# Optimization experiments

Hardware: AMD Instinct MI355X
Metric: run time of the kernel (lower is better)

The kernel has to match this reference:

```python
import jax, jax.numpy as jnp
import numpy as np

POOL = 7          # cf.pool_size
SR = 2            # roi_align sampling_ratio
LEVELS = [0, 1, 2, 3]
C = 192           # cf.end_filts
HC = 2            # cf.head_classes
RF = 1
N_ROIS = 1000
B = 4


def roi_align_2d(fmap, boxes, batch_inds, pool_size=POOL, sr=SR):
    """Bilinear RoIAlign. fmap [B,C,H,W]; boxes [N,4] = (y1,x1,y2,x2) in fmap pixel coords."""
    _, _, H, W = fmap.shape
    y1, x1, y2, x2 = boxes[:, 0], boxes[:, 1], boxes[:, 2], boxes[:, 3]
    bin_h = jnp.maximum(y2 - y1, 1.0) / pool_size
    bin_w = jnp.maximum(x2 - x1, 1.0) / pool_size
    # sampling offsets within the roi, [pool*sr]
    grid = (jnp.arange(pool_size, dtype=jnp.float32)[:, None]
            + (jnp.arange(sr, dtype=jnp.float32)[None, :] + 0.5) / sr).reshape(-1)
    ys = y1[:, None] + grid[None, :] * bin_h[:, None]   # [N, P*S]
    xs = x1[:, None] + grid[None, :] * bin_w[:, None]   # [N, P*S]
    y = jnp.broadcast_to(ys[:, :, None], (ys.shape[0], ys.shape[1], xs.shape[1]))  # [N,PS,PS]
    x = jnp.broadcast_to(xs[:, None, :], y.shape)
    valid = (y >= -1.0) & (y <= H) & (x >= -1.0) & (x <= W)
    y = jnp.clip(y, 0.0, H - 1)
    x = jnp.clip(x, 0.0, W - 1)
    y0 = jnp.floor(y).astype(jnp.int32)
    x0 = jnp.floor(x).astype(jnp.int32)
    y1i = jnp.minimum(y0 + 1, H - 1)
    x1i = jnp.minimum(x0 + 1, W - 1)
    ly = y - y0
    lx = x - x0
    b = batch_inds[:, None, None]
    f00 = fmap[b, :, y0, x0]    # [N,PS,PS,C]
    f01 = fmap[b, :, y0, x1i]
    f10 = fmap[b, :, y1i, x0]
    f11 = fmap[b, :, y1i, x1i]
    w00 = ((1 - ly) * (1 - lx))[..., None]
    w01 = ((1 - ly) * lx)[..., None]
    w10 = (ly * (1 - lx))[..., None]
    w11 = (ly * lx)[..., None]
    val = (f00 * w00 + f01 * w01 + f10 * w10 + f11 * w11) * valid[..., None]
    n = val.shape[0]
    val = val.reshape(n, pool_size, sr, pool_size, sr, -1).mean(axis=(2, 4))  # [N,P,P,C]
    return jnp.transpose(val, (0, 3, 1, 2))  # [N,C,P,P]


def pyramid_roi_align(fmaps, rois, pool_size=POOL, levels=LEVELS):
    boxes = jax.lax.stop_gradient(rois[:, :4])  # level_boxes.detach() in original
    batch_ix = rois[:, 4].astype(jnp.int32)
    h = boxes[:, 2] - boxes[:, 0]
    w = boxes[:, 3] - boxes[:, 1]
    roi_level = jnp.clip(jnp.round(4.0 + jnp.log2(jnp.sqrt(h * w))),
                         levels[0], levels[-1]).astype(jnp.int32)
    pooled = jnp.zeros((boxes.shape[0], fmaps[0].shape[1], pool_size, pool_size), fmaps[0].dtype)
    for li, lvl in enumerate(levels):
        H, W = fmaps[li].shape[2], fmaps[li].shape[3]
        scale = jnp.asarray([H, W, H, W], jnp.float32)
        p = roi_align_2d(fmaps[li], boxes * scale, batch_ix, pool_size)
        pooled = jnp.where((roi_level == lvl)[:, None, None, None], p, pooled)
    return pooled


def setup_inputs() -> dict:
    key = jax.random.key(0)
    ks = jax.random.split(key, 20)
    fmap0 = jax.random.normal(ks[0], (B, C, 128, 128), jnp.float32)
    fmap1 = jax.random.normal(ks[1], (B, C, 64, 64), jnp.float32)
    fmap2 = jax.random.normal(ks[2], (B, C, 32, 32), jnp.float32)
    fmap3 = jax.random.normal(ks[3], (B, C, 16, 16), jnp.float32)
    # valid normalized rois: (y1,x1,y2,x2,batch_ix)
    cy = jax.random.uniform(ks[4], (N_ROIS,), minval=0.15, maxval=0.85)
    cx = jax.random.uniform(ks[5], (N_ROIS,), minval=0.15, maxval=0.85)
    hh = jax.random.uniform(ks[6], (N_ROIS,), minval=0.02, maxval=0.15)
    hw = jax.random.uniform(ks[7], (N_ROIS,), minval=0.02, maxval=0.15)
    bix = jax.random.randint(ks[8], (N_ROIS,), 0, B).astype(jnp.float32)
    rois = jnp.stack([jnp.clip(cy - hh, 0, 1), jnp.clip(cx - hw, 0, 1),
                      jnp.clip(cy + hh, 0, 1), jnp.clip(cx + hw, 0, 1), bix], axis=1)
    d = C * 4  # 768
    s1 = 1.0 / np.sqrt(C * POOL * POOL)
    s2 = 1.0 / np.sqrt(d)
    params = dict(
        w1=jax.random.normal(ks[9], (d, C, POOL, POOL), jnp.float32) * s1,
        b1=jnp.zeros((d,), jnp.float32),
        w2=jax.random.normal(ks[10], (d, d), jnp.float32) * s2,
        b2=jnp.zeros((d,), jnp.float32),
        w_bbox=jax.random.normal(ks[11], (HC * 4, d), jnp.float32) * s2,
        b_bbox=jnp.zeros((HC * 4,), jnp.float32),
        w_cls=jax.random.normal(ks[12], (HC, d), jnp.float32) * s2,
        b_cls=jnp.zeros((HC,), jnp.float32),
        w_reg=jax.random.normal(ks[13], (HC * RF, d), jnp.float32) * s2,
        b_reg=jnp.zeros((HC * RF,), jnp.float32),
        w_unc=jax.random.normal(ks[14], (HC, d), jnp.float32) * s2,
        b_unc=jnp.zeros((HC,), jnp.float32),
    )
    return dict(fmap0=fmap0, fmap1=fmap1, fmap2=fmap2, fmap3=fmap3, rois=rois, **params)


def reference(fmap0, fmap1, fmap2, fmap3, rois, w1, b1, w2, b2,
              w_bbox, b_bbox, w_cls, b_cls, w_reg, b_reg, w_unc, b_unc):
    x = pyramid_roi_align([fmap0, fmap1, fmap2, fmap3], rois)      # [N,C,7,7]
    x = jax.nn.relu(jnp.einsum('ncij,ocij->no', x, w1) + b1)       # conv1 ks=7 -> 1x1
    x = jax.nn.relu(x @ w2.T + b2)                                 # conv2 1x1
    n = x.shape[0]
    mrcnn_bbox = (x @ w_bbox.T + b_bbox).reshape(n, -1, 4)         # [N,HC,2*dim]
    mrcnn_class_logits = x @ w_cls.T + b_cls                       # [N,HC]
    reg = (x @ w_reg.T + b_reg).reshape(n, -1, RF)
    unc = x @ w_unc.T + b_unc
    mrcnn_regress = jnp.concatenate([reg, unc[..., None]], axis=2)  # [N,HC,RF+1]
    return mrcnn_bbox, mrcnn_class_logits, mrcnn_regress
```

## Files before the change

kernel.cpp:

```cpp
#include <hip/hip_runtime.h>
#include <hip/hip_bf16.h>
#include <cstddef>
#include <cstdint>

typedef __attribute__((ext_vector_type(8))) short short8;
typedef __attribute__((ext_vector_type(16))) float float16;

#define C_CH 192
#define PK   9408
#define D1   768

__device__ __forceinline__ ushort f2bf(float v) {
    return __builtin_bit_cast(unsigned short, __float2bfloat16(v));
}

__global__ __launch_bounds__(256) void cvt_bf16_2(
    const float* __restrict__ in1, ushort* __restrict__ out1, int n4_1,
    const float* __restrict__ in2, ushort* __restrict__ out2, int n4_2)
{
    int i = blockIdx.x * 256 + threadIdx.x;
    const float* in; ushort* out;
    if (i < n4_1) { in = in1; out = out1; }
    else          { i -= n4_1; if (i >= n4_2) return; in = in2; out = out2; }
    float4 v = ((const float4*)in)[i];
    ushort4 o;
    o.x = f2bf(v.x); o.y = f2bf(v.y); o.z = f2bf(v.z); o.w = f2bf(v.w);
    ((ushort4*)out)[i] = o;
}

__global__ __launch_bounds__(256) void cvt_bf16(const float* __restrict__ in,
                                                ushort* __restrict__ out, int n4)
{
    int i = blockIdx.x * 256 + threadIdx.x;
    if (i >= n4) return;
    float4 v = ((const float4*)in)[i];
    ushort4 o;
    o.x = f2bf(v.x); o.y = f2bf(v.y); o.z = f2bf(v.z); o.w = f2bf(v.w);
    ((ushort4*)out)[i] = o;
}

__global__ __launch_bounds__(256) void fused_pre(
    const float* __restrict__ f0, const float* __restrict__ f1,
    const float* __restrict__ f2, const float* __restrict__ f3,
    ushort* __restrict__ o0, ushort* __restrict__ o1,
    ushort* __restrict__ o2, ushort* __restrict__ o3,
    const float* __restrict__ w1src, ushort* __restrict__ w1dst, int n41,
    const float* __restrict__ w2src, ushort* __restrict__ w2dst, int n42,
    int nTrans)
{
    __shared__ unsigned int sm[96][33];

    int bx = blockIdx.x;
    if (bx >= nTrans) {
        int i = (bx - nTrans) * 256 + threadIdx.x;
        const float* in; ushort* out;
        if (i < n41) { in = w1src; out = w1dst; }
        else         { i -= n41; if (i >= n42) return; in = w2src; out = w2dst; }
        float4 v = ((const float4*)in)[i];
        ushort4 o;
        o.x = f2bf(v.x); o.y = f2bf(v.y); o.z = f2bf(v.z); o.w = f2bf(v.w);
        ((ushort4*)out)[i] = o;
        return;
    }

    int b = bx / 680;
    int t = bx - b * 680;
    const float* in; ushort* out; int HW, hw0;
    if      (t < 512) { in = f0; out = o0; HW = 16384; hw0 = t * 32; }
    else if (t < 640) { in = f1; out = o1; HW = 4096;  hw0 = (t - 512) * 32; }
    else if (t < 672) { in = f2; out = o2; HW = 1024;  hw0 = (t - 640) * 32; }
    else              { in = f3; out = o3; HW = 256;   hw0 = (t - 672) * 32; }

    int tx = threadIdx.x & 31;
    int ty = threadIdx.x >> 5;

    const float* ip = in + (size_t)b * C_CH * HW + hw0;
    #pragma unroll
    for (int it = 0; it < 12; ++it) {
        int cp = it * 8 + ty;
        float v0 = ip[(size_t)(2 * cp)     * HW + tx];
        float v1 = ip[(size_t)(2 * cp + 1) * HW + tx];
        sm[cp][tx] = (unsigned int)f2bf(v0) | ((unsigned int)f2bf(v1) << 16);
    }
    __syncthreads();

    unsigned int* op = (unsigned int*)(out + ((size_t)b * HW + hw0) * C_CH);
    #pragma unroll
    for (int it = 0; it < 12; ++it) {
        int idx = it * 256 + (int)threadIdx.x;
        int r = idx / 96;
        int p = idx - r * 96;
        op[idx] = sm[p][r];
    }
}

__device__ __forceinline__ void issue8(
    const char* sbase, const int (*offB)[4], int s2, int c16, float4* u)
{
    #pragma unroll
    for (int k = 0; k < 8; ++k) {
        int s  = s2 + (k >> 2);
        int tp = k & 3;
        u[k] = *(const float4*)(sbase + (offB[s][tp] + c16));
    }
}

__device__ __forceinline__ void comp8(
    const float4* u, const float (*wt)[4], int s2, float* a)
{
    #pragma unroll
    for (int k = 0; k < 8; ++k) {
        float w = wt[s2 + (k >> 2)][k & 3];
        unsigned int u0 = __builtin_bit_cast(unsigned int, u[k].x);
        unsigned int u1 = __builtin_bit_cast(unsigned int, u[k].y);
        unsigned int u2 = __builtin_bit_cast(unsigned int, u[k].z);
        unsigned int u3 = __builtin_bit_cast(unsigned int, u[k].w);
        a[0] = fmaf(__builtin_bit_cast(float, u0 << 16),         w, a[0]);
        a[1] = fmaf(__builtin_bit_cast(float, u0 & 0xffff0000u), w, a[1]);
        a[2] = fmaf(__builtin_bit_cast(float, u1 << 16),         w, a[2]);
        a[3] = fmaf(__builtin_bit_cast(float, u1 & 0xffff0000u), w, a[3]);
        a[4] = fmaf(__builtin_bit_cast(float, u2 << 16),         w, a[4]);
        a[5] = fmaf(__builtin_bit_cast(float, u2 & 0xffff0000u), w, a[5]);
        a[6] = fmaf(__builtin_bit_cast(float, u3 << 16),         w, a[6]);
        a[7] = fmaf(__builtin_bit_cast(float, u3 & 0xffff0000u), w, a[7]);
    }
}

__global__ __launch_bounds__(384, 3) void roi_gather(
    const ushort* __restrict__ n0p, const ushort* __restrict__ n1p,
    const ushort* __restrict__ n2p, const ushort* __restrict__ n3p,
    const float* __restrict__ rois, ushort* __restrict__ pooled)
{
    __shared__ int    s_offB[196][4];
    __shared__ float  s_w[196][4];
    __shared__ ushort s_out[PK];

    const int n   = blockIdx.x;
    const int tid = threadIdx.x;

    float by1 = rois[n*5+0], bx1 = rois[n*5+1];
    float by2 = rois[n*5+2], bx2 = rois[n*5+3];
    int   b   = (int)rois[n*5+4];

    float hh = by2 - by1, ww = bx2 - bx1;
    int lvl = (int)rintf(4.0f + log2f(sqrtf(hh * ww)));
    lvl = min(max(lvl, 0), 3);

    const ushort* fm; int H;
    if      (lvl == 0) { fm = n0p; H = 128; }
    else if (lvl == 1) { fm = n1p; H = 64;  }
    else if (lvl == 2) { fm = n2p; H = 32;  }
    else               { fm = n3p; H = 16;  }
    float Hf = (float)H;

    float y1p = by1 * Hf, x1p = bx1 * Hf;
    float y2p = by2 * Hf, x2p = bx2 * Hf;
    float bin_h = fmaxf(y2p - y1p, 1.0f) * (1.0f / 7.0f);
    float bin_w = fmaxf(x2p - x1p, 1.0f) * (1.0f / 7.0f);

    uintptr_t bp = (uintptr_t)(fm + (size_t)b * H * H * C_CH);
    unsigned int blo = __builtin_amdgcn_readfirstlane((unsigned int)bp);
    unsigned int bhi = __builtin_amdgcn_readfirstlane((unsigned int)(bp >> 32));
    const char* sbase = (const char*)((((uintptr_t)bhi) << 32) | blo);

    if (tid < 196) {
        int s = tid;
        int sx = s & 1, sy = (s >> 1) & 1, ij = s >> 2;
        int i = ij / 7, j = ij - i * 7;

        float gy = (float)i + 0.25f + 0.5f * (float)sy;
        float y  = y1p + gy * bin_h;
        bool  vy = (y >= -1.0f) && (y <= Hf);
        float yc = fminf(fmaxf(y, 0.0f), Hf - 1.0f);
        int   y0 = (int)floorf(yc);
        float ly = yc - (float)y0;
        int   y1i = min(y0 + 1, H - 1);

        float gx = (float)j + 0.25f + 0.5f * (float)sx;
        float x  = x1p + gx * bin_w;
        bool  vx = (x >= -1.0f) && (x <= Hf);
        float xc = fminf(fmaxf(x, 0.0f), Hf - 1.0f);
        int   x0 = (int)floorf(xc);
        float lx = xc - (float)x0;
        int   x1i = min(x0 + 1, H - 1);

        float vm = (vy && vx) ? 0.25f : 0.0f;
        s_offB[s][0] = (y0  * H + x0 ) * (C_CH * 2);
        s_offB[s][1] = (y0  * H + x1i) * (C_CH * 2);
        s_offB[s][2] = (y1i * H + x0 ) * (C_CH * 2);
        s_offB[s][3] = (y1i * H + x1i) * (C_CH * 2);
        s_w[s][0] = (1.0f - ly) * (1.0f - lx) * vm;
        s_w[s][1] = (1.0f - ly) * lx * vm;
        s_w[s][2] = ly * (1.0f - lx) * vm;
        s_w[s][3] = ly * lx * vm;
    }
    __syncthreads();

    const int grp = tid / 24;
    const int ci  = tid - grp * 24;
    const int cl  = ci * 8;
    const int c16 = ci * 16;
    const int bin_lo = (grp * 49) >> 4;
    const int bin_hi = ((grp + 1) * 49) >> 4;

    float4 ua[8], ub[8];
    float  a[8];

    issue8(sbase, s_offB, bin_lo * 4, c16, ua);
    for (int bin = bin_lo; bin < bin_hi; ++bin) {
        issue8(sbase, s_offB, bin * 4 + 2, c16, ub);
        #pragma unroll
        for (int k = 0; k < 8; ++k) a[k] = 0.0f;
        comp8(ua, s_w, bin * 4, a);
        if (bin + 1 < bin_hi)
            issue8(sbase, s_offB, (bin + 1) * 4, c16, ua);
        comp8(ub, s_w, bin * 4 + 2, a);
        #pragma unroll
        for (int k = 0; k < 8; ++k)
            s_out[(cl + k) * 49 + bin] = f2bf(a[k]);
    }
    __syncthreads();

    unsigned int* po = (unsigned int*)(pooled + (size_t)n * PK);
    const unsigned int* so = (const unsigned int*)s_out;
    for (int idx = tid; idx < PK / 2; idx += 384) po[idx] = so[idx];
}

__global__ __launch_bounds__(256) void roi_align_nchw(
    const float* __restrict__ f0, const float* __restrict__ f1,
    const float* __restrict__ f2, const float* __restrict__ f3,
    const float* __restrict__ rois, ushort* __restrict__ pooled, int n_rois)
{
    int idx = blockIdx.x * 256 + threadIdx.x;
    if (idx >= n_rois * PK) return;
    int n  = idx / PK;
    int r  = idx - n * PK;
    int c  = r / 49;
    int ij = r - c * 49;
    int i  = ij / 7;
    int j  = ij - i * 7;

    float by1 = rois[n*5+0], bx1 = rois[n*5+1];
    float by2 = rois[n*5+2], bx2 = rois[n*5+3];
    int   b   = (int)rois[n*5+4];

    float hh = by2 - by1, ww = bx2 - bx1;
    int lvl = (int)rintf(4.0f + log2f(sqrtf(hh * ww)));
    lvl = min(max(lvl, 0), 3);

    const float* fmap; int H;
    if      (lvl == 0) { fmap = f0; H = 128; }
    else if (lvl == 1) { fmap = f1; H = 64;  }
    else if (lvl == 2) { fmap = f2; H = 32;  }
    else               { fmap = f3; H = 16;  }
    float Hf = (float)H;

    float y1p = by1 * Hf, x1p = bx1 * Hf;
    float bin_h = fmaxf(by2 * Hf - y1p, 1.0f) * (1.0f / 7.0f);
    float bin_w = fmaxf(bx2 * Hf - x1p, 1.0f) * (1.0f / 7.0f);

    const float* base = fmap + ((size_t)b * C_CH + c) * (size_t)(H * H);

    float acc = 0.0f;
    #pragma unroll
    for (int sy = 0; sy < 2; ++sy) {
        float y  = y1p + ((float)i + 0.25f + 0.5f * (float)sy) * bin_h;
        bool  vy = (y >= -1.0f) && (y <= Hf);
        float yc = fminf(fmaxf(y, 0.0f), Hf - 1.0f);
        int   y0 = (int)floorf(yc);
        float ly = yc - (float)y0;
        int   y1i = min(y0 + 1, H - 1);
        #pragma unroll
        for (int sx = 0; sx < 2; ++sx) {
            float x  = x1p + ((float)j + 0.25f + 0.5f * (float)sx) * bin_w;
            bool  vx = (x >= -1.0f) && (x <= Hf);
            float xc = fminf(fmaxf(x, 0.0f), Hf - 1.0f);
            int   x0 = (int)floorf(xc);
            float lx = xc - (float)x0;
            int   x1i = min(x0 + 1, H - 1);
            if (vy && vx) {
                float v = base[y0 * H + x0 ] * (1.0f - ly) * (1.0f - lx)
                        + base[y0 * H + x1i] * (1.0f - ly) * lx
                        + base[y1i * H + x0 ] * ly * (1.0f - lx)
                        + base[y1i * H + x1i] * ly * lx;
                acc += v;
            }
        }
    }
    pooled[idx] = f2bf(acc * 0.25f);
}

template<int MODE>
__global__ __launch_bounds__(256) void mfma_gemm(
    const ushort* __restrict__ A, const ushort* __restrict__ W,
    const float* __restrict__ bias, void* __restrict__ outp,
    int M, int N, int K, int nkPer, int nkTotal)
{
    __shared__ char ldsA[2][8192];
    __shared__ char ldsB[2][8192];

    const int t    = threadIdx.x;
    const int lane = t & 63;
    const int wave = t >> 6;
    const int wm = wave >> 1, wn = wave & 1;

    const int m0 = blockIdx.y * 64;
    const int n0 = blockIdx.x * 64;
    const int kb = (MODE == 2) ? blockIdx.z * nkPer : 0;
    const int nk = (MODE == 2) ? min(nkPer, nkTotal - kb) : nkPer;

    const int ks   = t & 3;
    const int mrow = t >> 2;
    const int g    = mrow >> 5;
    const int rw   = mrow & 31;
    const int lof0 = ks*2048 + g*1024 + ((     rw) ^ (ks<<2))*16;
    const int lof1 = ks*2048 + g*1024 + ((32 + rw) ^ (ks<<2))*16;

    const int arow = min(m0 + mrow, M-1);
    const int brow = n0 + mrow;
    const ushort* ap = A + (size_t)arow * K + (size_t)kb * 64 + ks*16;
    const ushort* bp = W + (size_t)brow * K + (size_t)kb * 64 + ks*16;

    float4 ra0, ra1, rb0, rb1;
    float4 qa0, qa1, qb0, qb1;

    ra0 = ((const float4*)ap)[0]; ra1 = ((const float4*)ap)[1];
    rb0 = ((const float4*)bp)[0]; rb1 = ((const float4*)bp)[1];
    *(float4*)&ldsA[0][lof0] = ra0; *(float4*)&ldsA[0][lof1] = ra1;
    *(float4*)&ldsB[0][lof0] = rb0; *(float4*)&ldsB[0][lof1] = rb1;
    {
        int k1 = min(1, nk - 1);
        const ushort* ap1 = ap + (size_t)k1 * 64;
        const ushort* bp1 = bp + (size_t)k1 * 64;
        ra0 = ((const float4*)ap1)[0]; ra1 = ((const float4*)ap1)[1];
        rb0 = ((const float4*)bp1)[0]; rb1 = ((const float4*)bp1)[1];
    }
    __syncthreads();

    float16 acc = {};

    for (int kt = 0; kt < nk; ++kt) {
        {
            int k2 = min(kt + 2, nk - 1);
            const ushort* ap2 = ap + (size_t)k2 * 64;
            const ushort* bp2 = bp + (size_t)k2 * 64;
            qa0 = ((const float4*)ap2)[0]; qa1 = ((const float4*)ap2)[1];
            qb0 = ((const float4*)bp2)[0]; qb1 = ((const float4*)bp2)[1];
        }
        if (kt + 1 < nk) {
            char* dA = ldsA[(kt+1)&1]; char* dB = ldsB[(kt+1)&1];
            *(float4*)&dA[lof0] = ra0; *(float4*)&dA[lof1] = ra1;
            *(float4*)&dB[lof0] = rb0; *(float4*)&dB[lof1] = rb1;
        }
        const char* sA = ldsA[kt&1]; const char* sB = ldsB[kt&1];
        #pragma unroll
        for (int s = 0; s < 4; ++s) {
            int ro = s*2048 + (lane ^ (s<<2))*16;
            short8 af = *(const short8*)&sA[wm*1024 + ro];
            short8 bf = *(const short8*)&sB[wn*1024 + ro];
            acc = __builtin_amdgcn_mfma_f32_32x32x16_bf16(af, bf, acc, 0, 0, 0);
        }
        __syncthreads();
        ra0 = qa0; ra1 = qa1; rb0 = qb0; rb1 = qb1;
    }

    const int col   = lane & 31;
    const int rbase = 4 * (lane >> 5);
    const int nG    = n0 + wn*32 + col;

    if (MODE == 2) {
        float* O = (float*)outp + (size_t)blockIdx.z * M * N;
        #pragma unroll
        for (int r = 0; r < 16; ++r) {
            int row = (r & 3) + 8*(r >> 2) + rbase;
            int mG  = m0 + wm*32 + row;
            if (mG < M) O[(size_t)mG * N + nG] = acc[r];
        }
    } else if (MODE == 1) {
        const float bv = bias[nG];
        ushort* O = (ushort*)outp;
        #pragma unroll
        for (int r = 0; r < 16; ++r) {
            int row = (r & 3) + 8*(r >> 2) + rbase;
            int mG  = m0 + wm*32 + row;
            if (mG < M) O[(size_t)mG * N + nG] = f2bf(fmaxf(acc[r] + bv, 0.0f));
        }
    } else {
        const float bv = bias[nG];
        float* O = (float*)outp;
        #pragma unroll
        for (int r = 0; r < 16; ++r) {
            int row = (r & 3) + 8*(r >> 2) + rbase;
            int mG  = m0 + wm*32 + row;
            if (mG < M) O[(size_t)mG * N + nG] = fmaxf(acc[r] + bv, 0.0f);
        }
    }
}

__global__ __launch_bounds__(256) void mfma_gemm128(
    const ushort* __restrict__ A, const ushort* __restrict__ W,
    void* __restrict__ outp, int M, int N, int K, int nkPer, int nkTotal)
{
    __shared__ char ldsA[2][16384];
    __shared__ char ldsB[2][16384];

    const int t    = threadIdx.x;
    const int lane = t & 63;
    const int wave = t >> 6;
    const int wm = wave >> 1, wn = wave & 1;

    const int m0 = blockIdx.y * 128;
    const int n0 = blockIdx.x * 128;
    const int kb = blockIdx.z * nkPer;
    const int nk = min(nkPer, nkTotal - kb);

    const int ks   = t & 3;
    const int mrow = t >> 2;
    const int g    = mrow >> 5;
    const int rw   = mrow & 31;
    const int swz  = ks << 2;
    const int lof0 = ks*4096 + g*1024 + ((     rw) ^ swz)*16;
    const int lof1 = ks*4096 + g*1024 + ((32 + rw) ^ swz)*16;

    const int arow0 = min(m0 + mrow,      M-1);
    const int arow1 = min(m0 + mrow + 64, M-1);
    const int brow0 = n0 + mrow;
    const int brow1 = n0 + mrow + 64;
    const ushort* ap0 = A + (size_t)arow0 * K + (size_t)kb * 64 + ks*16;
    const ushort* ap1 = A + (size_t)arow1 * K + (size_t)kb * 64 + ks*16;
    const ushort* bp0 = W + (size_t)brow0 * K + (size_t)kb * 64 + ks*16;
    const ushort* bp1 = W + (size_t)brow1 * K + (size_t)kb * 64 + ks*16;

    float4 ra0, ra1, ra2, ra3, rb0, rb1, rb2, rb3;
    float4 qa0, qa1, qa2, qa3, qb0, qb1, qb2, qb3;

    ra0 = ((const float4*)ap0)[0]; ra1 = ((const float4*)ap0)[1];
    ra2 = ((const float4*)ap1)[0]; ra3 = ((const float4*)ap1)[1];
    rb0 = ((const float4*)bp0)[0]; rb1 = ((const float4*)bp0)[1];
    rb2 = ((const float4*)bp1)[0]; rb3 = ((const float4*)bp1)[1];
    *(float4*)&ldsA[0][lof0]      = ra0; *(float4*)&ldsA[0][lof1]      = ra1;
    *(float4*)&ldsA[0][lof0+2048] = ra2; *(float4*)&ldsA[0][lof1+2048] = ra3;
    *(float4*)&ldsB[0][lof0]      = rb0; *(float4*)&ldsB[0][lof1]      = rb1;
    *(float4*)&ldsB[0][lof0+2048] = rb2; *(float4*)&ldsB[0][lof1+2048] = rb3;
    {
        int k1 = min(1, nk - 1);
        const ushort* a0 = ap0 + (size_t)k1 * 64; const ushort* a1 = ap1 + (size_t)k1 * 64;
        const ushort* b0 = bp0 + (size_t)k1 * 64; const ushort* b1 = bp1 + (size_t)k1 * 64;
        ra0 = ((const float4*)a0)[0]; ra1 = ((const float4*)a0)[1];
        ra2 = ((const float4*)a1)[0]; ra3 = ((const float4*)a1)[1];
        rb0 = ((const float4*)b0)[0]; rb1 = ((const float4*)b0)[1];
        rb2 = ((const float4*)b1)[0]; rb3 = ((const float4*)b1)[1];
    }
    __syncthreads();

    float16 acc00 = {}, acc01 = {}, acc10 = {}, acc11 = {};

    for (int kt = 0; kt < nk; ++kt) {
        {
            int k2 = min(kt + 2, nk - 1);
            const ushort* a0 = ap0 + (size_t)k2 * 64; const ushort* a1 = ap1 + (size_t)k2 * 64;
            const ushort* b0 = bp0 + (size_t)k2 * 64; const ushort* b1 = bp1 + (size_t)k2 * 64;
            qa0 = ((const float4*)a0)[0]; qa1 = ((const float4*)a0)[1];
            qa2 = ((const float4*)a1)[0]; qa3 = ((const float4*)a1)[1];
            qb0 = ((const float4*)b0)[0]; qb1 = ((const float4*)b0)[1];
            qb2 = ((const float4*)b1)[0]; qb3 = ((const float4*)b1)[1];
        }
        if (kt + 1 < nk) {
            char* dA = ldsA[(kt+1)&1]; char* dB = ldsB[(kt+1)&1];
            *(float4*)&dA[lof0]      = ra0; *(float4*)&dA[lof1]      = ra1;
            *(float4*)&dA[lof0+2048] = ra2; *(float4*)&dA[lof1+2048] = ra3;
            *(float4*)&dB[lof0]      = rb0; *(float4*)&dB[lof1]      = rb1;
            *(float4*)&dB[lof0+2048] = rb2; *(float4*)&dB[lof1+2048] = rb3;
        }
        const char* sA = ldsA[kt&1]; const char* sB = ldsB[kt&1];
        #pragma unroll
        for (int s = 0; s < 4; ++s) {
            int ro = s*4096 + (lane ^ (s<<2))*16;
            short8 a0 = *(const short8*)&sA[wm*2048        + ro];
            short8 a1 = *(const short8*)&sA[wm*2048 + 1024 + ro];
            short8 b0 = *(const short8*)&sB[wn*2048        + ro];
            short8 b1 = *(const short8*)&sB[wn*2048 + 1024 + ro];
            acc00 = __builtin_amdgcn_mfma_f32_32x32x16_bf16(a0, b0, acc00, 0, 0, 0);
            acc01 = __builtin_amdgcn_mfma_f32_32x32x16_bf16(a0, b1, acc01, 0, 0, 0);
            acc10 = __builtin_amdgcn_mfma_f32_32x32x16_bf16(a1, b0, acc10, 0, 0, 0);
            acc11 = __builtin_amdgcn_mfma_f32_32x32x16_bf16(a1, b1, acc11, 0, 0, 0);
        }
        __syncthreads();
        ra0 = qa0; ra1 = qa1; ra2 = qa2; ra3 = qa3;
        rb0 = qb0; rb1 = qb1; rb2 = qb2; rb3 = qb3;
    }

    const int col   = lane & 31;
    const int rbase = 4 * (lane >> 5);
    float* O = (float*)outp + (size_t)blockIdx.z * M * N;

    const int mb0 = m0 + wm*64;
    const int nb0 = n0 + wn*64;
    #pragma unroll
    for (int r = 0; r < 16; ++r) {
        int row = (r & 3) + 8*(r >> 2) + rbase;
        int mG0 = mb0 + row;
        int mG1 = mb0 + 32 + row;
        int nG0 = nb0 + col;
        int nG1 = nb0 + 32 + col;
        if (mG0 < M) {
            O[(size_t)mG0 * N + nG0] = acc00[r];
            O[(size_t)mG0 * N + nG1] = acc01[r];
        }
        if (mG1 < M) {
            O[(size_t)mG1 * N + nG0] = acc10[r];
            O[(size_t)mG1 * N + nG1] = acc11[r];
        }
    }
}

__global__ __launch_bounds__(256) void reduce_relu_bf16(
    const float* __restrict__ P, const float* __restrict__ bias,
    ushort* __restrict__ Y, int MN, int N, int S)
{
    int idx = blockIdx.x * 256 + threadIdx.x;
    if (idx >= MN / 4) return;
    float4 s = ((const float4*)P)[idx];
    for (int k = 1; k < S; ++k) {
        float4 p = ((const float4*)(P + (size_t)k * MN))[idx];
        s.x += p.x; s.y += p.y; s.z += p.z; s.w += p.w;
    }
    int n4 = idx % (N / 4);
    float4 bv = ((const float4*)bias)[n4];
    ushort4 o;
    o.x = f2bf(fmaxf(s.x + bv.x, 0.0f));
    o.y = f2bf(fmaxf(s.y + bv.y, 0.0f));
    o.z = f2bf(fmaxf(s.z + bv.z, 0.0f));
    o.w = f2bf(fmaxf(s.w + bv.w, 0.0f));
    ((ushort4*)Y)[idx] = o;
}

__global__ __launch_bounds__(256) void reduce_heads(
    const float* __restrict__ P2, const float* __restrict__ b2, int S, int MN,
    const float* __restrict__ w_bbox, const float* __restrict__ b_bbox,
    const float* __restrict__ w_cls,  const float* __restrict__ b_cls,
    const float* __restrict__ w_reg,  const float* __restrict__ b_reg,
    const float* __restrict__ w_unc,  const float* __restrict__ b_unc,
    float* __restrict__ out, int n_rois)
{
    __shared__ float zrow[D1];
    const int m   = blockIdx.x;
    const int tid = threadIdx.x;

    const float* Pm = P2 + (size_t)m * D1;
    #pragma unroll
    for (int r = 0; r < 3; ++r) {
        int k = r * 256 + tid;
        float v = Pm[k];
        for (int s = 1; s < S; ++s) v += Pm[(size_t)s * MN + k];
        zrow[k] = fmaxf(v + b2[k], 0.0f);
    }
    __syncthreads();

    const int wave = tid >> 6;
    const int lane = tid & 63;
    for (int o = wave; o < 14; o += 4) {
        const float* w; float bb;
        if      (o < 8)  { w = w_bbox + o * D1;        bb = b_bbox[o]; }
        else if (o < 10) { w = w_cls  + (o - 8) * D1;  bb = b_cls[o - 8]; }
        else if (o < 12) { w = w_reg  + (o - 10) * D1; bb = b_reg[o - 10]; }
        else             { w = w_unc  + (o - 12) * D1; bb = b_unc[o - 12]; }
        float p = 0.0f;
        #pragma unroll
        for (int r = 0; r < 12; ++r) {
            int k = r * 64 + lane;
            p = fmaf(zrow[k], w[k], p);
        }
        #pragma unroll
        for (int d = 32; d >= 1; d >>= 1) p += __shfl_down(p, d, 64);
        if (lane == 0) {
            int off;
            int clsOff = n_rois * 8;
            int regOff = n_rois * 10;
            if      (o < 8)  off = m * 8 + o;
            else if (o < 10) off = clsOff + m * 2 + (o - 8);
            else if (o < 12) off = regOff + m * 4 + (o - 10) * 2;
            else             off = regOff + m * 4 + (o - 12) * 2 + 1;
            out[off] = p + bb;
        }
    }
}

__global__ __launch_bounds__(256) void heads_kernel(
    const float* __restrict__ Z,
    const float* __restrict__ w_bbox, const float* __restrict__ b_bbox,
    const float* __restrict__ w_cls,  const float* __restrict__ b_cls,
    const float* __restrict__ w_reg,  const float* __restrict__ b_reg,
    const float* __restrict__ w_unc,  const float* __restrict__ b_unc,
    float* __restrict__ out, int n_rois)
{
    int idx = blockIdx.x * 256 + threadIdx.x;
    if (idx >= n_rois * 14) return;
    int n = idx / 14;
    int o = idx - n * 14;

    const float* w; float bb;
    if      (o < 8)  { w = w_bbox + o * D1;        bb = b_bbox[o]; }
    else if (o < 10) { w = w_cls  + (o - 8) * D1;  bb = b_cls[o - 8]; }
    else if (o < 12) { w = w_reg  + (o - 10) * D1; bb = b_reg[o - 10]; }
    else             { w = w_unc  + (o - 12) * D1; bb = b_unc[o - 12]; }

    const float* z = Z + (size_t)n * D1;
    float s = bb;
    for (int k = 0; k < D1; k += 4) {
        float4 zv = *(const float4*)(z + k);
        float4 wv = *(const float4*)(w + k);
        s = fmaf(zv.x, wv.x, s);
        s = fmaf(zv.y, wv.y, s);
        s = fmaf(zv.z, wv.z, s);
        s = fmaf(zv.w, wv.w, s);
    }

    int off;
    int clsOff = n_rois * 8;
    int regOff = n_rois * 10;
    if      (o < 8)  off = n * 8 + o;
    else if (o < 10) off = clsOff + n * 2 + (o - 8);
    else if (o < 12) off = regOff + n * 4 + (o - 10) * 2;
    else             off = regOff + n * 4 + (o - 12) * 2 + 1;
    out[off] = s;
}

extern "C" void kernel_launch(void* const* d_in, const int* in_sizes, int n_in,
                              void* d_out, int out_size, void* d_ws, size_t ws_size,
                              hipStream_t stream)
{
    const float* f0   = (const float*)d_in[0];
    const float* f1   = (const float*)d_in[1];
    const float* f2   = (const float*)d_in[2];
    const float* f3   = (const float*)d_in[3];
    const float* rois = (const float*)d_in[4];
    const float* w1   = (const float*)d_in[5];
    const float* b1   = (const float*)d_in[6];
    const float* w2   = (const float*)d_in[7];
    const float* b2   = (const float*)d_in[8];
    const float* w_bbox = (const float*)d_in[9];
    const float* b_bbox = (const float*)d_in[10];
    const float* w_cls  = (const float*)d_in[11];
    const float* b_cls  = (const float*)d_in[12];
    const float* w_reg  = (const float*)d_in[13];
    const float* b_reg  = (const float*)d_in[14];
    const float* w_unc  = (const float*)d_in[15];
    const float* b_unc  = (const float*)d_in[16];
    float* out = (float*)d_out;

    const int n_rois = in_sizes[4] / 5;
    const int B      = in_sizes[0] / (C_CH * 128 * 128);

    const size_t nh0B = (size_t)B * 16384 * C_CH * 2;
    const size_t nh1B = (size_t)B * 4096  * C_CH * 2;
    const size_t nh2B = (size_t)B * 1024  * C_CH * 2;
    const size_t nh3B = (size_t)B * 256   * C_CH * 2;
    const size_t nhAll = nh0B + nh1B + nh2B + nh3B;
    const size_t poolB = (size_t)n_rois * PK * 2;
    const size_t w1Bb  = (size_t)D1 * PK * 2;
    const size_t w2Bb  = (size_t)D1 * D1 * 2;
    const size_t Yb    = (size_t)n_rois * D1 * 2;
    const size_t Zb    = (size_t)n_rois * D1 * 4;
    const size_t smallB = w2Bb + Yb + Zb;

    const int SPLIT1  = 10;
    const int SPLIT1F = 5;
    const int SPLIT2  = 2;

    const size_t P1b   = (size_t)SPLIT1 * n_rois * D1 * 4;
    const size_t needX2 = nhAll + poolB + w1Bb + w2Bb + Yb;
    const size_t needX  = nhAll + poolB + smallB;

    char* ws = (char*)d_ws;

    int n41 = D1*PK/4, n42 = D1*D1/4;

    if (ws_size >= needX2) {
        ushort* nh0 = (ushort*)ws;
        ushort* nh1 = nh0 + nh0B/2;
        ushort* nh2 = nh1 + nh1B/2;
        ushort* nh3 = nh2 + nh2B/2;
        ushort* pooledB = (ushort*)(ws + nhAll);
        ushort* w1B = (ushort*)(ws + nhAll + poolB);
        ushort* w2B = (ushort*)(ws + nhAll + poolB + w1Bb);
        ushort* Y   = (ushort*)(ws + nhAll + poolB + w1Bb + w2Bb);
        float*  P   = (float*)ws;
        float*  P2  = (float*)(ws + P1b);

        int nTrans = 680 * B;
        int nCvt   = (n41 + n42 + 255) / 256;
        fused_pre<<<nTrans + nCvt, 256, 0, stream>>>(
            f0, f1, f2, f3, nh0, nh1, nh2, nh3,
            w1, w1B, n41, w2, w2B, n42, nTrans);

        roi_gather<<<n_rois, 384, 0, stream>>>(nh0, nh1, nh2, nh3, rois, pooledB);

        {
            int nkTotal = PK / 64;
            int nkPer   = (nkTotal + SPLIT1 - 1) / SPLIT1;
            dim3 grid(D1/128, (n_rois + 127)/128, SPLIT1);
            mfma_gemm128<<<grid, 256, 0, stream>>>(pooledB, w1B, P,
                                                   n_rois, D1, PK, nkPer, nkTotal);
            int MN = n_rois * D1;
            reduce_relu_bf16<<<(MN/4 + 255)/256, 256, 0, stream>>>(P, b1, Y, MN, D1, SPLIT1);
        }
        {
            int nkTotal = D1 / 64;
            int nkPer   = nkTotal / SPLIT2;
            dim3 grid(D1/64, (n_rois + 63)/64, SPLIT2);
            mfma_gemm<2><<<grid, 256, 0, stream>>>(Y, w2B, nullptr, P2,
                                                   n_rois, D1, D1, nkPer, nkTotal);
            int MN = n_rois * D1;
            reduce_heads<<<n_rois, 256, 0, stream>>>(P2, b2, SPLIT2, MN,
                w_bbox, b_bbox, w_cls, b_cls, w_reg, b_reg, w_unc, b_unc, out, n_rois);
        }
    } else if (ws_size >= needX) {
        ushort* nh0 = (ushort*)ws;
        ushort* nh1 = nh0 + nh0B/2;
        ushort* nh2 = nh1 + nh1B/2;
        ushort* nh3 = nh2 + nh2B/2;
        ushort* w1B = (ushort*)ws;
        float*  P   = (float*)(ws + w1Bb);
        float*  P2  = (float*)ws;
        ushort* pooledB = (ushort*)(ws + nhAll);
        ushort* w2B = (ushort*)(ws + nhAll + poolB);
        ushort* Y   = w2B + w2Bb/2;

        int nTrans = 680 * B;
        fused_pre<<<nTrans, 256, 0, stream>>>(
            f0, f1, f2, f3, nh0, nh1, nh2, nh3,
            w1, (ushort*)nullptr, 0, w2, (ushort*)nullptr, 0, nTrans);
        roi_gather<<<n_rois, 384, 0, stream>>>(nh0, nh1, nh2, nh3, rois, pooledB);
        cvt_bf16_2<<<(n41 + n42 + 255)/256, 256, 0, stream>>>(
            w1, w1B, n41, w2, w2B, n42);
        {
            int nkTotal = PK / 64;
            int nkPer   = (nkTotal + SPLIT1F - 1) / SPLIT1F;
            dim3 grid(D1/64, (n_rois + 63)/64, SPLIT1F);
            mfma_gemm<2><<<grid, 256, 0, stream>>>(pooledB, w1B, nullptr, P,
                                                   n_rois, D1, PK, nkPer, nkTotal);
            int MN = n_rois * D1;
            reduce_relu_bf16<<<(MN/4 + 255)/256, 256, 0, stream>>>(P, b1, Y, MN, D1, SPLIT1F);
        }
        {
            int nkTotal = D1 / 64;
            int nkPer   = nkTotal / SPLIT2;
            dim3 grid(D1/64, (n_rois + 63)/64, SPLIT2);
            mfma_gemm<2><<<grid, 256, 0, stream>>>(Y, w2B, nullptr, P2,
                                                   n_rois, D1, D1, nkPer, nkTotal);
            int MN = n_rois * D1;
            reduce_heads<<<n_rois, 256, 0, stream>>>(P2, b2, SPLIT2, MN,
                w_bbox, b_bbox, w_cls, b_cls, w_reg, b_reg, w_unc, b_unc, out, n_rois);
        }
    } else {
        ushort* pooledB = (ushort*)ws;
        ushort* w1B = pooledB + poolB/2;
        ushort* w2B = w1B + w1Bb/2;
        ushort* Y   = w2B + w2Bb/2;
        float*  Z   = (float*)((char*)Y + Yb);

        cvt_bf16<<<((D1*PK/4) + 255)/256, 256, 0, stream>>>(w1, w1B, D1*PK/4);
        cvt_bf16<<<((D1*D1/4) + 255)/256, 256, 0, stream>>>(w2, w2B, D1*D1/4);
        {
            int total = n_rois * PK;
            roi_align_nchw<<<(total + 255)/256, 256, 0, stream>>>(
                f0, f1, f2, f3, rois, pooledB, n_rois);
        }
        {
            dim3 grid(D1/64, (n_rois + 63)/64);
            mfma_gemm<1><<<grid, 256, 0, stream>>>(pooledB, w1B, b1, Y,
                                                   n_rois, D1, PK, PK/64, PK/64);
        }
        {
            dim3 grid(D1/64, (n_rois + 63)/64);
            mfma_gemm<0><<<grid, 256, 0, stream>>>(Y, w2B, b2, Z,
                                                   n_rois, D1, D1, D1/64, D1/64);
        }
        heads_kernel<<<(n_rois*14 + 255)/256, 256, 0, stream>>>(
            Z, w_bbox, b_bbox, w_cls, b_cls, w_reg, b_reg, w_unc, b_unc, out, n_rois);
    }
}
```

Baseline: 229.3 us.

## Stage GEMM tiles directly into LDS with global_load_lds instead of registers

Replaces the register-staged prefetch (global load into VGPRs, then a store to LDS) in the 128x128 MFMA GEMM with direct global-to-LDS 16-byte loads, keeping the swizzled layout through per-lane address remapping. This frees the prefetch registers and removes the explicit LDS store instructions. It drops the two-stage register lookahead, so only one tile is in flight ahead of compute. The loads also rely on the barrier to cover async completion, which risks exposing more memory latency.

```diff
diff --git a/kernel.cpp b/kernel.cpp
--- a/kernel.cpp
+++ b/kernel.cpp
@@ -12,6 +12,12 @@
 
 __device__ __forceinline__ ushort f2bf(float v) {
     return __builtin_bit_cast(unsigned short, __float2bfloat16(v));
+}
+
+__device__ __forceinline__ void gload16(const void* g, void* l) {
+    __builtin_amdgcn_global_load_lds(
+        (const __attribute__((address_space(1))) void*)g,
+        (__attribute__((address_space(3))) void*)l, 16, 0, 0);
 }
 
 __global__ __launch_bounds__(256) void cvt_bf16_2(
@@ -414,65 +420,42 @@
     const int kb = blockIdx.z * nkPer;
     const int nk = min(nkPer, nkTotal - kb);
 
-    const int ks   = t & 3;
-    const int mrow = t >> 2;
-    const int g    = mrow >> 5;
-    const int rw   = mrow & 31;
-    const int swz  = ks << 2;
-    const int lof0 = ks*4096 + g*1024 + ((     rw) ^ swz)*16;
-    const int lof1 = ks*4096 + g*1024 + ((32 + rw) ^ swz)*16;
-
-    const int arow0 = min(m0 + mrow,      M-1);
-    const int arow1 = min(m0 + mrow + 64, M-1);
-    const int brow0 = n0 + mrow;
-    const int brow1 = n0 + mrow + 64;
-    const ushort* ap0 = A + (size_t)arow0 * K + (size_t)kb * 64 + ks*16;
-    const ushort* ap1 = A + (size_t)arow1 * K + (size_t)kb * 64 + ks*16;
-    const ushort* bp0 = W + (size_t)brow0 * K + (size_t)kb * 64 + ks*16;
-    const ushort* bp1 = W + (size_t)brow1 * K + (size_t)kb * 64 + ks*16;
-
-    float4 ra0, ra1, ra2, ra3, rb0, rb1, rb2, rb3;
-    float4 qa0, qa1, qa2, qa3, qb0, qb1, qb2, qb3;
-
-    ra0 = ((const float4*)ap0)[0]; ra1 = ((const float4*)ap0)[1];
-    ra2 = ((const float4*)ap1)[0]; ra3 = ((const float4*)ap1)[1];
-    rb0 = ((const float4*)bp0)[0]; rb1 = ((const float4*)bp0)[1];
-    rb2 = ((const float4*)bp1)[0]; rb3 = ((const float4*)bp1)[1];
-    *(float4*)&ldsA[0][lof0]      = ra0; *(float4*)&ldsA[0][lof1]      = ra1;
-    *(float4*)&ldsA[0][lof0+2048] = ra2; *(float4*)&ldsA[0][lof1+2048] = ra3;
-    *(float4*)&ldsB[0][lof0]      = rb0; *(float4*)&ldsB[0][lof1]      = rb1;
-    *(float4*)&ldsB[0][lof0+2048] = rb2; *(float4*)&ldsB[0][lof1+2048] = rb3;
-    {
-        int k1 = min(1, nk - 1);
-        const ushort* a0 = ap0 + (size_t)k1 * 64; const ushort* a1 = ap1 + (size_t)k1 * 64;
-        const ushort* b0 = bp0 + (size_t)k1 * 64; const ushort* b1 = bp1 + (size_t)k1 * 64;
-        ra0 = ((const float4*)a0)[0]; ra1 = ((const float4*)a0)[1];
-        ra2 = ((const float4*)a1)[0]; ra3 = ((const float4*)a1)[1];
-        rb0 = ((const float4*)b0)[0]; rb1 = ((const float4*)b0)[1];
-        rb2 = ((const float4*)b1)[0]; rb3 = ((const float4*)b1)[1];
-    }
+    int aoff[4], boff[4], lofs[4];
+    #pragma unroll
+    for (int i = 0; i < 4; ++i) {
+        int sid = wave * 4 + i;
+        int ks = sid >> 2, h = (sid >> 1) & 1, g = sid & 1;
+        int swz = ks << 2;
+        int rl  = h * 64 + g * 32 + ((lane & 31) ^ swz);
+        int ko  = ks * 16 + (lane >> 5) * 8;
+        int arow = min(m0 + rl, M - 1);
+        int brow = n0 + rl;
+        aoff[i] = arow * K + ko;
+        boff[i] = brow * K + ko;
+        lofs[i] = sid * 1024;
+    }
+    const size_t kbase = (size_t)kb * 64;
+
+    #define STAGE128(buf, kt)                                                  \
+        do {                                                                   \
+            const ushort* Ab_ = A + kbase + (size_t)(kt) * 64;                 \
+            const ushort* Wb_ = W + kbase + (size_t)(kt) * 64;                 \
+            _Pragma("unroll")                                                  \
+            for (int i_ = 0; i_ < 4; ++i_) {                                   \
+                gload16(Ab_ + aoff[i_], &ldsA[buf][lofs[i_]]);                 \
+                gload16(Wb_ + boff[i_], &ldsB[buf][lofs[i_]]);                 \
+            }                                                                  \
+        } while (0)
+
+    STAGE128(0, 0);
     __syncthreads();
 
     float16 acc00 = {}, acc01 = {}, acc10 = {}, acc11 = {};
 
     for (int kt = 0; kt < nk; ++kt) {
-        {
-            int k2 = min(kt + 2, nk - 1);
-            const ushort* a0 = ap0 + (size_t)k2 * 64; const ushort* a1 = ap1 + (size_t)k2 * 64;
-            const ushort* b0 = bp0 + (size_t)k2 * 64; const ushort* b1 = bp1 + (size_t)k2 * 64;
-            qa0 = ((const float4*)a0)[0]; qa1 = ((const float4*)a0)[1];
-            qa2 = ((const float4*)a1)[0]; qa3 = ((const float4*)a1)[1];
-            qb0 = ((const float4*)b0)[0]; qb1 = ((const float4*)b0)[1];
-            qb2 = ((const float4*)b1)[0]; qb3 = ((const float4*)b1)[1];
-        }
-        if (kt + 1 < nk) {
-            char* dA = ldsA[(kt+1)&1]; char* dB = ldsB[(kt+1)&1];
-            *(float4*)&dA[lof0]      = ra0; *(float4*)&dA[lof1]      = ra1;
-            *(float4*)&dA[lof0+2048] = ra2; *(float4*)&dA[lof1+2048] = ra3;
-            *(float4*)&dB[lof0]      = rb0; *(float4*)&dB[lof1]      = rb1;
-            *(float4*)&dB[lof0+2048] = rb2; *(float4*)&dB[lof1+2048] = rb3;
-        }
-        const char* sA = ldsA[kt&1]; const char* sB = ldsB[kt&1];
+        if (kt + 1 < nk) STAGE128((kt + 1) & 1, kt + 1);
+        const char* sA = ldsA[kt & 1];
+        const char* sB = ldsB[kt & 1];
         #pragma unroll
         for (int s = 0; s < 4; ++s) {
             int ro = s*4096 + (lane ^ (s<<2))*16;
@@ -486,9 +469,8 @@
             acc11 = __builtin_amdgcn_mfma_f32_32x32x16_bf16(a1, b1, acc11, 0, 0, 0);
         }
         __syncthreads();
-        ra0 = qa0; ra1 = qa1; ra2 = qa2; ra3 = qa3;
-        rb0 = qb0; rb1 = qb1; rb2 = qb2; rb3 = qb3;
-    }
+    }
+    #undef STAGE128
 
     const int col   = lane & 31;
     const int rbase = 4 * (lane >> 5);
```

New measurement: 229.4 us. Within noise of the previous version (+0.0%).
